# Performance work log

Hardware: AMD Instinct MI355X
Metric: run time of the kernel (lower is better)

## Reference

```python
import jax, jax.numpy as jnp
import numpy as np

B, S, D, H = 4, 1024, 2048, 16
DK = D // H
SPARSITY = 0.3


def setup_inputs() -> dict:
    key = jax.random.key(0)
    ks = jax.random.split(key, 9)
    scale = 0.02
    return {
        "x": jax.random.normal(ks[0], (B, S, D), dtype=jnp.float32),
        "Wq": jax.random.normal(ks[1], (D, D), dtype=jnp.float32) * scale,
        "bq": jnp.zeros((D,), dtype=jnp.float32),
        "Wk": jax.random.normal(ks[2], (D, D), dtype=jnp.float32) * scale,
        "bk": jnp.zeros((D,), dtype=jnp.float32),
        "Wv": jax.random.normal(ks[3], (D, D), dtype=jnp.float32) * scale,
        "bv": jnp.zeros((D,), dtype=jnp.float32),
        "Wo": jax.random.normal(ks[4], (D, D), dtype=jnp.float32) * scale,
        "bo": jnp.zeros((D,), dtype=jnp.float32),
    }


def reference(x, Wq, bq, Wk, bk, Wv, bv, Wo, bo):
    b, s, d = x.shape
    h, dk = H, d // H
    # projections (torch Linear: x @ W.T + b), split heads -> [b,h,s,dk]
    q = (x @ Wq.T + bq).reshape(b, s, h, dk).transpose(0, 2, 1, 3)
    k = (x @ Wk.T + bk).reshape(b, s, h, dk).transpose(0, 2, 1, 3)
    v = (x @ Wv.T + bv).reshape(b, s, h, dk).transpose(0, 2, 1, 3)
    scores = jnp.einsum("bhqd,bhkd->bhqk", q, k) / jnp.sqrt(jnp.float32(dk))
    kk = max(1, int(s * SPARSITY))
    top_vals, top_idx = jax.lax.top_k(scores, kk)  # [b,h,s,kk]
    # scatter top-k scores into -inf background (matches torch scatter_ on full_like(-inf))
    sparse = jnp.put_along_axis(
        jnp.full_like(scores, -jnp.inf), top_idx, top_vals, axis=-1, inplace=False
    )
    attn = jax.nn.softmax(sparse, axis=-1)  # each row has kk finite entries
    out = jnp.einsum("bhqk,bhkd->bhqd", attn, v)
    out = out.transpose(0, 2, 1, 3).reshape(b, s, d)
    out = out @ Wo.T + bo
    return out, attn
```

## Files before the change

kernel.cpp:

```cpp
#include <hip/hip_runtime.h>
#include <math.h>

#define BB 4
#define SS 1024
#define DD 2048
#define HH 16
#define DKK 128
#define KKTOP 307
#define MROWS (BB * SS)
#define KPLANE ((size_t)MROWS * DD)
static __device__ __constant__ float SCALE = 0.08838834764831845f;

typedef float f32x4 __attribute__((ext_vector_type(4)));
typedef unsigned short su4 __attribute__((ext_vector_type(4)));
typedef unsigned short su8 __attribute__((ext_vector_type(8)));

__device__ __forceinline__ unsigned short f2bf(float x) {
    unsigned u = __float_as_uint(x);
    u += 0x7fffu + ((u >> 16) & 1u);
    return (unsigned short)(u >> 16);
}
__device__ __forceinline__ float bf2f(unsigned short b) {
    return __uint_as_float((unsigned)b << 16);
}
__device__ __forceinline__ unsigned f2u_ord(float f) {
    unsigned x = __float_as_uint(f);
    return (x & 0x80000000u) ? ~x : (x | 0x80000000u);
}
__device__ __forceinline__ float u2f_ord(unsigned u) {
    return __uint_as_float((u & 0x80000000u) ? (u & 0x7fffffffu) : ~u);
}
__device__ __forceinline__ void split4(float4 v, su4& a, su4& b, su4& c) {
    float x[4] = {v.x, v.y, v.z, v.w};
    #pragma unroll
    for (int i = 0; i < 4; ++i) {
        unsigned short b1 = f2bf(x[i]);
        float r = x[i] - bf2f(b1);
        unsigned short b2 = f2bf(r);
        float r2 = r - bf2f(b2);
        a[i] = b1; b[i] = b2; c[i] = f2bf(r2);
    }
}
__device__ __forceinline__ void split2_4(float4 v, su4& a, su4& b) {
    float x[4] = {v.x, v.y, v.z, v.w};
    #pragma unroll
    for (int i = 0; i < 4; ++i) {
        unsigned short b1 = f2bf(x[i]);
        float r = x[i] - bf2f(b1);
        a[i] = b1; b[i] = f2bf(r);
    }
}
__device__ __forceinline__ su8 cat44(su4 a, su4 b) {
    su8 r;
    r[0] = a[0]; r[1] = a[1]; r[2] = a[2]; r[3] = a[3];
    r[4] = b[0]; r[5] = b[1]; r[6] = b[2]; r[7] = b[3];
    return r;
}

#define TM 128
#define TN 128

#define G3LD 40

__global__ __launch_bounds__(256) void gemm_nt_3p(
    const float* __restrict__ A, const float* __restrict__ W,
    const float* __restrict__ bias, float* __restrict__ C,
    int M, int N, int K)
{
    __shared__ unsigned short A1[128][G3LD];
    __shared__ unsigned short A2[128][G3LD];
    __shared__ unsigned short B1[128][G3LD];
    __shared__ unsigned short B2[128][G3LD];

    const int tid = threadIdx.x;
    const int bm = blockIdx.x * 128;
    const int bn = blockIdx.y * 128;
    const int wm = (tid >> 6) & 1;
    const int wn = tid >> 7;
    const int lane = tid & 63;
    const int lrow = tid >> 1;
    const int lcol = (tid & 1) * 16;

    f32x4 acc[4][4];
    #pragma unroll
    for (int i = 0; i < 4; ++i)
        #pragma unroll
        for (int j = 0; j < 4; ++j)
            acc[i][j] = (f32x4){0.f, 0.f, 0.f, 0.f};

    for (int kt = 0; kt < K; kt += 32) {
        __syncthreads();
        {
            const float* Ag = A + (size_t)(bm + lrow) * K + kt + lcol;
            const float* Wg = W + (size_t)(bn + lrow) * K + kt + lcol;
            float4 v0, v1; su4 h0, l0, h1, l1;
            v0 = *(const float4*)(Ag + 0);  v1 = *(const float4*)(Ag + 4);
            split2_4(v0, h0, l0); split2_4(v1, h1, l1);
            *(su8*)&A1[lrow][lcol + 0] = cat44(h0, h1);
            *(su8*)&A2[lrow][lcol + 0] = cat44(l0, l1);
            v0 = *(const float4*)(Ag + 8);  v1 = *(const float4*)(Ag + 12);
            split2_4(v0, h0, l0); split2_4(v1, h1, l1);
            *(su8*)&A1[lrow][lcol + 8] = cat44(h0, h1);
            *(su8*)&A2[lrow][lcol + 8] = cat44(l0, l1);
            v0 = *(const float4*)(Wg + 0);  v1 = *(const float4*)(Wg + 4);
            split2_4(v0, h0, l0); split2_4(v1, h1, l1);
            *(su8*)&B1[lrow][lcol + 0] = cat44(h0, h1);
            *(su8*)&B2[lrow][lcol + 0] = cat44(l0, l1);
            v0 = *(const float4*)(Wg + 8);  v1 = *(const float4*)(Wg + 12);
            split2_4(v0, h0, l0); split2_4(v1, h1, l1);
            *(su8*)&B1[lrow][lcol + 8] = cat44(h0, h1);
            *(su8*)&B2[lrow][lcol + 8] = cat44(l0, l1);
        }
        __syncthreads();

        su8 a1[4], a2[4], b1[4], b2[4];
        #pragma unroll
        for (int f = 0; f < 4; ++f) {
            const int fr = f * 16 + (lane & 15);
            const int fk = (lane >> 4) * 8;
            a1[f] = *(const su8*)&A1[wm * 64 + fr][fk];
            a2[f] = *(const su8*)&A2[wm * 64 + fr][fk];
            b1[f] = *(const su8*)&B1[wn * 64 + fr][fk];
            b2[f] = *(const su8*)&B2[wn * 64 + fr][fk];
        }
        #pragma unroll
        for (int fi = 0; fi < 4; ++fi)
            #pragma unroll
            for (int fj = 0; fj < 4; ++fj) {
                asm volatile("v_mfma_f32_16x16x32_bf16 %0, %1, %2, %0"
                             : "+v"(acc[fi][fj]) : "v"(a1[fi]), "v"(b2[fj]));
                asm volatile("v_mfma_f32_16x16x32_bf16 %0, %1, %2, %0"
                             : "+v"(acc[fi][fj]) : "v"(a2[fi]), "v"(b1[fj]));
                asm volatile("v_mfma_f32_16x16x32_bf16 %0, %1, %2, %0"
                             : "+v"(acc[fi][fj]) : "v"(a1[fi]), "v"(b1[fj]));
            }
    }

    asm volatile("s_nop 7\n\ts_nop 7" ::: "memory");

    #pragma unroll
    for (int fj = 0; fj < 4; ++fj) {
        const int col = bn + wn * 64 + fj * 16 + (lane & 15);
        const float bv = bias[col];
        #pragma unroll
        for (int fi = 0; fi < 4; ++fi) {
            const int r0 = bm + wm * 64 + fi * 16 + (lane >> 4) * 4;
            #pragma unroll
            for (int j = 0; j < 4; ++j)
                C[(size_t)(r0 + j) * N + col] = acc[fi][fj][j] + bv;
        }
    }
}

__global__ __launch_bounds__(256) void gemm_nt_3p_ksplit(
    const float* __restrict__ A, const float* __restrict__ W,
    const float* __restrict__ bias, unsigned short* __restrict__ Ks,
    int M, int N, int K)
{
    __shared__ unsigned short A1[128][G3LD];
    __shared__ unsigned short A2[128][G3LD];
    __shared__ unsigned short B1[128][G3LD];
    __shared__ unsigned short B2[128][G3LD];

    const int tid = threadIdx.x;
    const int bm = blockIdx.x * 128;
    const int bn = blockIdx.y * 128;
    const int wm = (tid >> 6) & 1;
    const int wn = tid >> 7;
    const int lane = tid & 63;
    const int lrow = tid >> 1;
    const int lcol = (tid & 1) * 16;

    f32x4 acc[4][4];
    #pragma unroll
    for (int i = 0; i < 4; ++i)
        #pragma unroll
        for (int j = 0; j < 4; ++j)
            acc[i][j] = (f32x4){0.f, 0.f, 0.f, 0.f};

    for (int kt = 0; kt < K; kt += 32) {
        __syncthreads();
        {
            const float* Ag = A + (size_t)(bm + lrow) * K + kt + lcol;
            const float* Wg = W + (size_t)(bn + lrow) * K + kt + lcol;
            float4 v0, v1; su4 h0, l0, h1, l1;
            v0 = *(const float4*)(Ag + 0);  v1 = *(const float4*)(Ag + 4);
            split2_4(v0, h0, l0); split2_4(v1, h1, l1);
            *(su8*)&A1[lrow][lcol + 0] = cat44(h0, h1);
            *(su8*)&A2[lrow][lcol + 0] = cat44(l0, l1);
            v0 = *(const float4*)(Ag + 8);  v1 = *(const float4*)(Ag + 12);
            split2_4(v0, h0, l0); split2_4(v1, h1, l1);
            *(su8*)&A1[lrow][lcol + 8] = cat44(h0, h1);
            *(su8*)&A2[lrow][lcol + 8] = cat44(l0, l1);
            v0 = *(const float4*)(Wg + 0);  v1 = *(const float4*)(Wg + 4);
            split2_4(v0, h0, l0); split2_4(v1, h1, l1);
            *(su8*)&B1[lrow][lcol + 0] = cat44(h0, h1);
            *(su8*)&B2[lrow][lcol + 0] = cat44(l0, l1);
            v0 = *(const float4*)(Wg + 8);  v1 = *(const float4*)(Wg + 12);
            split2_4(v0, h0, l0); split2_4(v1, h1, l1);
            *(su8*)&B1[lrow][lcol + 8] = cat44(h0, h1);
            *(su8*)&B2[lrow][lcol + 8] = cat44(l0, l1);
        }
        __syncthreads();

        su8 a1[4], a2[4], b1[4], b2[4];
        #pragma unroll
        for (int f = 0; f < 4; ++f) {
            const int fr = f * 16 + (lane & 15);
            const int fk = (lane >> 4) * 8;
            a1[f] = *(const su8*)&A1[wm * 64 + fr][fk];
            a2[f] = *(const su8*)&A2[wm * 64 + fr][fk];
            b1[f] = *(const su8*)&B1[wn * 64 + fr][fk];
            b2[f] = *(const su8*)&B2[wn * 64 + fr][fk];
        }
        #pragma unroll
        for (int fi = 0; fi < 4; ++fi)
            #pragma unroll
            for (int fj = 0; fj < 4; ++fj) {
                asm volatile("v_mfma_f32_16x16x32_bf16 %0, %1, %2, %0"
                             : "+v"(acc[fi][fj]) : "v"(a1[fi]), "v"(b2[fj]));
                asm volatile("v_mfma_f32_16x16x32_bf16 %0, %1, %2, %0"
                             : "+v"(acc[fi][fj]) : "v"(a2[fi]), "v"(b1[fj]));
                asm volatile("v_mfma_f32_16x16x32_bf16 %0, %1, %2, %0"
                             : "+v"(acc[fi][fj]) : "v"(a1[fi]), "v"(b1[fj]));
            }
    }

    asm volatile("s_nop 7\n\ts_nop 7" ::: "memory");

    #pragma unroll
    for (int fj = 0; fj < 4; ++fj) {
        const int col = bn + wn * 64 + fj * 16 + (lane & 15);
        const int h = col >> 7, d = col & (DKK - 1);
        const float bv = bias[col];
        #pragma unroll
        for (int fi = 0; fi < 4; ++fi) {
            const int r0 = bm + wm * 64 + fi * 16 + (lane >> 4) * 4;
            #pragma unroll
            for (int j = 0; j < 4; ++j) {
                const int tok = r0 + j;
                const float val = acc[fi][fj][j] + bv;
                const size_t o = ((size_t)((tok >> 10) * HH + h) * SS
                                  + (tok & (SS - 1))) * DKK + d;
                unsigned short s1 = f2bf(val);
                float r = val - bf2f(s1);
                unsigned short s2 = f2bf(r);
                float r2 = r - bf2f(s2);
                Ks[0 * KPLANE + o] = s1;
                Ks[1 * KPLANE + o] = s2;
                Ks[2 * KPLANE + o] = f2bf(r2);
            }
        }
    }
}

#define GLDA 40

__device__ __forceinline__ su8 pack8(float4 x, float4 y) {
    su8 r;
    r[0] = f2bf(x.x); r[1] = f2bf(x.y); r[2] = f2bf(x.z); r[3] = f2bf(x.w);
    r[4] = f2bf(y.x); r[5] = f2bf(y.y); r[6] = f2bf(y.z); r[7] = f2bf(y.w);
    return r;
}

__global__ __launch_bounds__(256) void gemm_nt_bf16(
    const float* __restrict__ A, const float* __restrict__ W,
    const float* __restrict__ bias, float* __restrict__ C,
    int M, int N, int K)
{
    __shared__ unsigned short Ab[128][GLDA];
    __shared__ unsigned short Bb[128][GLDA];

    const int tid = threadIdx.x;
    const int bm = blockIdx.x * 128;
    const int bn = blockIdx.y * 128;
    const int wm = (tid >> 6) & 1;
    const int wn = tid >> 7;
    const int lane = tid & 63;
    const int lrow = tid >> 1;
    const int lcol = (tid & 1) * 16;

    f32x4 acc[4][4];
    #pragma unroll
    for (int i = 0; i < 4; ++i)
        #pragma unroll
        for (int j = 0; j < 4; ++j)
            acc[i][j] = (f32x4){0.f, 0.f, 0.f, 0.f};

    for (int kt = 0; kt < K; kt += 32) {
        __syncthreads();
        {
            const float* Ag = A + (size_t)(bm + lrow) * K + kt + lcol;
            const float* Wg = W + (size_t)(bn + lrow) * K + kt + lcol;
            float4 a0 = *(const float4*)(Ag + 0);
            float4 a1 = *(const float4*)(Ag + 4);
            float4 a2 = *(const float4*)(Ag + 8);
            float4 a3 = *(const float4*)(Ag + 12);
            *(su8*)&Ab[lrow][lcol + 0] = pack8(a0, a1);
            *(su8*)&Ab[lrow][lcol + 8] = pack8(a2, a3);
            float4 b0 = *(const float4*)(Wg + 0);
            float4 b1 = *(const float4*)(Wg + 4);
            float4 b2 = *(const float4*)(Wg + 8);
            float4 b3 = *(const float4*)(Wg + 12);
            *(su8*)&Bb[lrow][lcol + 0] = pack8(b0, b1);
            *(su8*)&Bb[lrow][lcol + 8] = pack8(b2, b3);
        }
        __syncthreads();

        su8 af[4], bf[4];
        #pragma unroll
        for (int f = 0; f < 4; ++f) {
            af[f] = *(const su8*)&Ab[wm * 64 + f * 16 + (lane & 15)][(lane >> 4) * 8];
            bf[f] = *(const su8*)&Bb[wn * 64 + f * 16 + (lane & 15)][(lane >> 4) * 8];
        }
        #pragma unroll
        for (int fi = 0; fi < 4; ++fi)
            #pragma unroll
            for (int fj = 0; fj < 4; ++fj)
                asm volatile("v_mfma_f32_16x16x32_bf16 %0, %1, %2, %0"
                             : "+v"(acc[fi][fj])
                             : "v"(af[fi]), "v"(bf[fj]));
    }

    asm volatile("s_nop 7\n\ts_nop 7" ::: "memory");

    #pragma unroll
    for (int fj = 0; fj < 4; ++fj) {
        const int col = bn + wn * 64 + fj * 16 + (lane & 15);
        const float bv = bias[col];
        #pragma unroll
        for (int fi = 0; fi < 4; ++fi) {
            const int r0 = bm + wm * 64 + fi * 16 + (lane >> 4) * 4;
            #pragma unroll
            for (int j = 0; j < 4; ++j)
                C[(size_t)(r0 + j) * N + col] = acc[fi][fj][j] + bv;
        }
    }
}

__global__ __launch_bounds__(256) void gemm_nt_bf16_tv(
    const float* __restrict__ A, const float* __restrict__ W,
    const float* __restrict__ bias, unsigned short* __restrict__ Cb,
    int M, int N, int K)
{
    __shared__ unsigned short Ab[128][GLDA];
    __shared__ unsigned short Bb[128][GLDA];

    const int tid = threadIdx.x;
    const int bm = blockIdx.x * 128;
    const int bn = blockIdx.y * 128;
    const int wm = (tid >> 6) & 1;
    const int wn = tid >> 7;
    const int lane = tid & 63;
    const int lrow = tid >> 1;
    const int lcol = (tid & 1) * 16;

    f32x4 acc[4][4];
    #pragma unroll
    for (int i = 0; i < 4; ++i)
        #pragma unroll
        for (int j = 0; j < 4; ++j)
            acc[i][j] = (f32x4){0.f, 0.f, 0.f, 0.f};

    for (int kt = 0; kt < K; kt += 32) {
        __syncthreads();
        {
            const float* Ag = A + (size_t)(bm + lrow) * K + kt + lcol;
            const float* Wg = W + (size_t)(bn + lrow) * K + kt + lcol;
            float4 a0 = *(const float4*)(Ag + 0);
            float4 a1 = *(const float4*)(Ag + 4);
            float4 a2 = *(const float4*)(Ag + 8);
            float4 a3 = *(const float4*)(Ag + 12);
            *(su8*)&Ab[lrow][lcol + 0] = pack8(a0, a1);
            *(su8*)&Ab[lrow][lcol + 8] = pack8(a2, a3);
            float4 b0 = *(const float4*)(Wg + 0);
            float4 b1 = *(const float4*)(Wg + 4);
            float4 b2 = *(const float4*)(Wg + 8);
            float4 b3 = *(const float4*)(Wg + 12);
            *(su8*)&Bb[lrow][lcol + 0] = pack8(b0, b1);
            *(su8*)&Bb[lrow][lcol + 8] = pack8(b2, b3);
        }
        __syncthreads();

        su8 af[4], bf[4];
        #pragma unroll
        for (int f = 0; f < 4; ++f) {
            af[f] = *(const su8*)&Ab[wm * 64 + f * 16 + (lane & 15)][(lane >> 4) * 8];
            bf[f] = *(const su8*)&Bb[wn * 64 + f * 16 + (lane & 15)][(lane >> 4) * 8];
        }
        #pragma unroll
        for (int fi = 0; fi < 4; ++fi)
            #pragma unroll
            for (int fj = 0; fj < 4; ++fj)
                asm volatile("v_mfma_f32_16x16x32_bf16 %0, %1, %2, %0"
                             : "+v"(acc[fi][fj])
                             : "v"(af[fi]), "v"(bf[fj]));
    }

    asm volatile("s_nop 7\n\ts_nop 7" ::: "memory");

    #pragma unroll
    for (int fj = 0; fj < 4; ++fj) {
        const int col = bn + wn * 64 + fj * 16 + (lane & 15);
        #pragma unroll
        for (int fi = 0; fi < 4; ++fi) {
            const int r0 = bm + wm * 64 + fi * 16 + (lane >> 4) * 4;
            #pragma unroll
            for (int j = 0; j < 4; ++j) {
                float v = acc[fi][fj][j] + bias[r0 + j];
                Cb[(size_t)(r0 + j) * N + col] = f2bf(v);
            }
        }
    }
}

#define ATT_LDS 65280

__global__ __launch_bounds__(512) void attn_topk_fused(
    const float* __restrict__ Qb, const unsigned short* __restrict__ Ks,
    const unsigned short* __restrict__ Vt, float* __restrict__ attn_out,
    float* __restrict__ CTX)
{
    __shared__ __align__(16) char smem[ATT_LDS];
    unsigned short* q_s = (unsigned short*)smem;
    unsigned short* k_s = (unsigned short*)(smem + 13056);
    float*          red = (float*)smem;
    unsigned short* wt  = (unsigned short*)(smem + 13056);
    unsigned short* vt  = (unsigned short*)(smem + 13056 + 33024);

    const int tid = threadIdx.x;
    const int wv = tid >> 6, lane = tid & 63;
    const int fg = lane >> 4, fc = lane & 15;

    const int gg = (blockIdx.x & 7) * 512 + ((int)blockIdx.x >> 3);
    const int bh = gg >> 6, qb = gg & 63;
    const int b = bh >> 4, h = bh & 15;
    const int q0 = qb * 16;

    const float* Qg = Qb + (size_t)(b * SS + q0) * DD + h * DKK;
    const unsigned short* Ksg = Ks + (size_t)bh * SS * DKK;
    const unsigned short* Vtg = Vt + (size_t)(h * DKK) * MROWS + b * SS;
    float* aob = attn_out + (size_t)(bh * SS + q0) * SS;

    {
        int row = tid >> 5, c4 = tid & 31;
        float4 v = *(const float4*)(Qg + (size_t)row * DD + c4 * 4);
        int off = row * 136 + c4 * 4;
        su4 p1, p2, p3; split4(v, p1, p2, p3);
        *(su4*)&q_s[off] = p1;
        *(su4*)&q_s[2176 + off] = p2;
        *(su4*)&q_s[4352 + off] = p3;
    }
    __syncthreads();

    const int kt0 = (wv >> 2) * 2;
    su8 af[3][2];
    #pragma unroll
    for (int p = 0; p < 3; ++p)
        #pragma unroll
        for (int kk = 0; kk < 2; ++kk)
            af[p][kk] = *(const su8*)&q_s[p * 2176 + fc * 136 +
                            ((kt0 + kk) * 4 + fg) * 8];

    for (int t = 0; t < 16; ++t) {
        #pragma unroll
        for (int pu = 0; pu < 6; ++pu) {
            const int p = pu >> 1;
            const int rem = tid + 512 * (pu & 1);
            const int row = rem >> 4, c8 = rem & 15;
            su8 v = *(const su8*)(Ksg + p * KPLANE +
                                  (size_t)(t * 64 + row) * DKK + c8 * 8);
            *(su8*)&k_s[p * 8704 + row * 136 + c8 * 8] = v;
        }
        __syncthreads();

        const int krow = (wv & 3) * 16 + fc;
        su8 bf[3][2];
        #pragma unroll
        for (int p = 0; p < 3; ++p)
            #pragma unroll
            for (int kk = 0; kk < 2; ++kk)
                bf[p][kk] = *(const su8*)&k_s[p * 8704 + krow * 136 +
                                ((kt0 + kk) * 4 + fg) * 8];

        f32x4 acc = {0.f, 0.f, 0.f, 0.f};
        constexpr int PI[6] = {2, 0, 1, 1, 0, 0};
        constexpr int PJ[6] = {0, 2, 1, 0, 1, 0};
        #pragma unroll
        for (int p = 0; p < 6; ++p)
            #pragma unroll
            for (int kk = 0; kk < 2; ++kk)
                asm volatile("v_mfma_f32_16x16x32_bf16 %0, %1, %2, %0"
                             : "+v"(acc) : "v"(af[PI[p]][kk]), "v"(bf[PJ[p]][kk]));
        asm volatile("s_nop 7\n\ts_nop 7" ::: "memory");

        if (kt0 == 2) {
            #pragma unroll
            for (int j = 0; j < 4; ++j)
                red[(wv & 3) * 256 + (4 * fg + j) * 16 + fc] = acc[j];
        }
        __syncthreads();
        if (kt0 == 0) {
            #pragma unroll
            for (int j = 0; j < 4; ++j) {
                float s = (acc[j] + red[(wv & 3) * 256 + (4 * fg + j) * 16 + fc]) * SCALE;
                aob[(size_t)(4 * fg + j) * SS + t * 64 + (wv & 3) * 16 + fc] = s;
            }
        }
        __syncthreads();
    }
    __syncthreads();

    unsigned uv[2][16];
    #pragma unroll
    for (int rr = 0; rr < 2; ++rr) {
        const float* aor = aob + (size_t)(2 * wv + rr) * SS;
        #pragma unroll
        for (int t = 0; t < 16; ++t)
            uv[rr][t] = f2u_ord(aor[t * 64 + lane]);
    }
    unsigned pref[2]; int ecnt[2]; float mrow[2], invz[2], tvexp[2];
    #pragma unroll
    for (int rr = 0; rr < 2; ++rr) {
        unsigned p = 0;
        for (int bit = 31; bit >= 0; --bit) {
            unsigned cand = p | (1u << bit);
            int cnt = 0;
            #pragma unroll
            for (int t = 0; t < 16; ++t)
                cnt += __popcll(__ballot(uv[rr][t] >= cand));
            if (cnt >= KKTOP) p = cand;
        }
        pref[rr] = p;
        int g = 0;
        #pragma unroll
        for (int t = 0; t < 16; ++t)
            g += __popcll(__ballot(uv[rr][t] > p));
        ecnt[rr] = KKTOP - g;

        unsigned um = 0;
        #pragma unroll
        for (int t = 0; t < 16; ++t) um = um > uv[rr][t] ? um : uv[rr][t];
        #pragma unroll
        for (int o = 32; o > 0; o >>= 1) {
            unsigned tv2 = __shfl_down(um, o);
            um = um > tv2 ? um : tv2;
        }
        um = __shfl(um, 0);
        const float m = u2f_ord(um);

        float se = 0.f;
        #pragma unroll
        for (int t = 0; t < 16; ++t)
            if (uv[rr][t] > p) se += expf(u2f_ord(uv[rr][t]) - m);
        #pragma unroll
        for (int o = 32; o > 0; o >>= 1) se += __shfl_down(se, o);
        se = __shfl(se, 0);

        mrow[rr] = m;
        tvexp[rr] = expf(u2f_ord(p) - m);
        invz[rr] = 1.0f / (se + (float)ecnt[rr] * tvexp[rr]);
    }

    #pragma unroll
    for (int rr = 0; rr < 2; ++rr) {
        float* aor = aob + (size_t)(2 * wv + rr) * SS;
        unsigned short* wr = wt + (2 * wv + rr) * 1032;
        int tiesbefore = 0;
        #pragma unroll
        for (int t = 0; t < 16; ++t) {
            const unsigned u = uv[rr][t];
            const bool eq = (u == pref[rr]);
            unsigned long long mask = __ballot(eq);
            float w;
            if (u > pref[rr]) {
                w = expf(u2f_ord(u) - mrow[rr]) * invz[rr];
            } else if (eq) {
                int rank = tiesbefore + __popcll(mask & ((1ull << lane) - 1ull));
                w = (rank < ecnt[rr]) ? tvexp[rr] * invz[rr] : 0.f;
            } else {
                w = 0.f;
            }
            aor[t * 64 + lane] = w;
            wr[t * 64 + lane] = f2bf(w);
            tiesbefore += __popcll(mask);
        }
    }

    f32x4 pacc = {0.f, 0.f, 0.f, 0.f};
    const int pvd = wv * 16 + fc;
    for (int t = 0; t < 16; ++t) {
        __syncthreads();
        #pragma unroll
        for (int u = 0; u < 2; ++u) {
            int rem = tid + 512 * u;
            int d = rem >> 3, kc = rem & 7;
            su8 v = *(const su8*)(Vtg + (size_t)d * MROWS + t * 64 + kc * 8);
            *(su8*)&vt[d * 72 + kc * 8] = v;
        }
        __syncthreads();
        #pragma unroll
        for (int kk = 0; kk < 2; ++kk) {
            su8 aw = *(const su8*)&wt[fc * 1032 + t * 64 + (kk * 4 + fg) * 8];
            su8 bv2 = *(const su8*)&vt[pvd * 72 + (kk * 4 + fg) * 8];
            asm volatile("v_mfma_f32_16x16x32_bf16 %0, %1, %2, %0"
                         : "+v"(pacc) : "v"(aw), "v"(bv2));
        }
    }
    asm volatile("s_nop 7\n\ts_nop 7" ::: "memory");

    #pragma unroll
    for (int j = 0; j < 4; ++j)
        CTX[(size_t)(b * SS + q0 + 4 * fg + j) * DD + h * DKK + pvd] = pacc[j];
}

extern "C" void kernel_launch(void* const* d_in, const int* in_sizes, int n_in,
                              void* d_out, int out_size, void* d_ws, size_t ws_size,
                              hipStream_t stream)
{
    const float* x  = (const float*)d_in[0];
    const float* Wq = (const float*)d_in[1];
    const float* bq = (const float*)d_in[2];
    const float* Wk = (const float*)d_in[3];
    const float* bk = (const float*)d_in[4];
    const float* Wv = (const float*)d_in[5];
    const float* bv = (const float*)d_in[6];
    const float* Wo = (const float*)d_in[7];
    const float* bo = (const float*)d_in[8];

    float* out      = (float*)d_out;
    float* attn_out = (float*)d_out + (size_t)MROWS * DD;

    float* ws = (float*)d_ws;
    const size_t PLANE = (size_t)MROWS * DD;
    float* Qb = ws;
    unsigned short* Ksp = (unsigned short*)(ws + PLANE);
    float* CTX = ws + PLANE + PLANE * 3 / 2;
    unsigned short* Vtp = (unsigned short*)(ws + PLANE + PLANE * 3 / 2 + PLANE);

    dim3 gb(MROWS / TM, DD / TN);
    gemm_nt_3p<<<gb, 256, 0, stream>>>(x, Wq, bq, Qb, MROWS, DD, DD);
    gemm_nt_3p_ksplit<<<gb, 256, 0, stream>>>(x, Wk, bk, Ksp, MROWS, DD, DD);
    gemm_nt_bf16_tv<<<dim3(DD / TM, MROWS / TN), 256, 0, stream>>>(
        Wv, x, bv, Vtp, DD, MROWS, DD);

    attn_topk_fused<<<dim3(BB * HH * (SS / 16)), 512, 0, stream>>>(
        Qb, Ksp, Vtp, attn_out, CTX);

    gemm_nt_bf16<<<gb, 256, 0, stream>>>(CTX, Wo, bo, out, MROWS, DD, DD);
}
```

Before: 1.082 ms.

## Prefetch next K and V tiles into registers during attention loops

The QK^T and PV loops now load the next iteration's K and V tiles from global memory into registers while the current tile is consumed from shared memory. This overlaps global-load latency with MFMA work. A redundant trailing barrier in the score loop is also removed, since the top-of-loop barrier already orders the shared-memory reuse. The cost is extra VGPRs for the staged tiles, which could lower occupancy.

```diff
diff --git a/kernel.cpp b/kernel.cpp
--- a/kernel.cpp
+++ b/kernel.cpp
@@ -442,6 +442,16 @@
     const unsigned short* Vtg = Vt + (size_t)(h * DKK) * MROWS + b * SS;
     float* aob = attn_out + (size_t)(bh * SS + q0) * SS;
 
+    su8 rk[6];
+    #pragma unroll
+    for (int pu = 0; pu < 6; ++pu) {
+        const int p = pu >> 1;
+        const int rem = tid + 512 * (pu & 1);
+        const int row = rem >> 4, c8 = rem & 15;
+        rk[pu] = *(const su8*)(Ksg + p * KPLANE +
+                               (size_t)row * DKK + c8 * 8);
+    }
+
     {
         int row = tid >> 5, c4 = tid & 31;
         float4 v = *(const float4*)(Qg + (size_t)row * DD + c4 * 4);
@@ -468,9 +478,17 @@
             const int p = pu >> 1;
             const int rem = tid + 512 * (pu & 1);
             const int row = rem >> 4, c8 = rem & 15;
-            su8 v = *(const su8*)(Ksg + p * KPLANE +
-                                  (size_t)(t * 64 + row) * DKK + c8 * 8);
-            *(su8*)&k_s[p * 8704 + row * 136 + c8 * 8] = v;
+            *(su8*)&k_s[p * 8704 + row * 136 + c8 * 8] = rk[pu];
+        }
+        if (t < 15) {
+            #pragma unroll
+            for (int pu = 0; pu < 6; ++pu) {
+                const int p = pu >> 1;
+                const int rem = tid + 512 * (pu & 1);
+                const int row = rem >> 4, c8 = rem & 15;
+                rk[pu] = *(const su8*)(Ksg + p * KPLANE +
+                            (size_t)((t + 1) * 64 + row) * DKK + c8 * 8);
+            }
         }
         __syncthreads();
 
@@ -507,7 +525,6 @@
                 aob[(size_t)(4 * fg + j) * SS + t * 64 + (wv & 3) * 16 + fc] = s;
             }
         }
-        __syncthreads();
     }
     __syncthreads();
 
@@ -589,14 +606,29 @@
 
     f32x4 pacc = {0.f, 0.f, 0.f, 0.f};
     const int pvd = wv * 16 + fc;
+    su8 rv[2];
+    #pragma unroll
+    for (int u = 0; u < 2; ++u) {
+        int rem = tid + 512 * u;
+        int d = rem >> 3, kc = rem & 7;
+        rv[u] = *(const su8*)(Vtg + (size_t)d * MROWS + kc * 8);
+    }
     for (int t = 0; t < 16; ++t) {
         __syncthreads();
         #pragma unroll
         for (int u = 0; u < 2; ++u) {
             int rem = tid + 512 * u;
             int d = rem >> 3, kc = rem & 7;
-            su8 v = *(const su8*)(Vtg + (size_t)d * MROWS + t * 64 + kc * 8);
-            *(su8*)&vt[d * 72 + kc * 8] = v;
+            *(su8*)&vt[d * 72 + kc * 8] = rv[u];
+        }
+        if (t < 15) {
+            #pragma unroll
+            for (int u = 0; u < 2; ++u) {
+                int rem = tid + 512 * u;
+                int d = rem >> 3, kc = rem & 7;
+                rv[u] = *(const su8*)(Vtg + (size_t)d * MROWS +
+                                      (t + 1) * 64 + kc * 8);
+            }
         }
         __syncthreads();
         #pragma unroll
```

Result: faster. 983.5 us (-9.1%).
